# Kernel tuning notes

Measured on AMD Instinct MI355X. Metric: run time of the kernel, lower is better.

The kernel has to match this reference:

```python
import jax, jax.numpy as jnp
import numpy as np

N = 50000   # nodes
E = 800000  # edges (avg degree 16)
D = 256     # input = hidden = output dim
L = 3       # num_layers


def setup_inputs() -> dict:
    key = jax.random.key(0)
    k0, k1, k2, k3 = jax.random.split(key, 4)
    x = jax.random.normal(k0, (N, D), dtype=jnp.float32)
    edge_index = jax.random.randint(k1, (2, E), 0, N, dtype=jnp.int32)
    # SAGEConv params per layer: lin_l (neighbor path, with bias), lin_r (root path)
    Wl = jax.random.normal(k2, (L, D, D), dtype=jnp.float32) * 0.05
    Wr = jax.random.normal(k3, (L, D, D), dtype=jnp.float32) * 0.05
    b = jnp.zeros((L, D), dtype=jnp.float32)
    return {"x": x, "edge_index": edge_index, "Wl": Wl, "Wr": Wr, "b": b}


def reference(x, edge_index, Wl, Wr, b):
    src = edge_index[0]
    dst = edge_index[1]
    # in-degree for mean aggregation (clamped to avoid div-by-zero)
    deg = jax.ops.segment_sum(jnp.ones((E,), x.dtype), dst, num_segments=N)
    inv_deg = (1.0 / jnp.maximum(deg, 1.0))[:, None]  # [N,1]
    h = x
    for i in range(L):
        # gather source features, scatter-add into destinations, then mean
        agg = jax.ops.segment_sum(h[src], dst, num_segments=N) * inv_deg  # [N,D]
        h = agg @ Wl[i] + h @ Wr[i] + b[i]
        if i < L - 1:
            h = jax.nn.relu(h)  # dropout(p=0.1) is identity in eval mode
    return h
```

## Files before the change

### kernel.cpp

```cpp
#include <hip/hip_runtime.h>


typedef __attribute__((ext_vector_type(8))) _Float16 f16x8;
typedef __attribute__((ext_vector_type(4))) float f32x4;

__global__ void count_deg_kernel(const int* __restrict__ dst,
                                 int* __restrict__ deg, int E) {
    int i = (blockIdx.x * blockDim.x + threadIdx.x) * 2;
    if (i + 1 < E) {
        int2 d = *(const int2*)&dst[i];
        atomicAdd(&deg[d.x], 1);
        atomicAdd(&deg[d.y], 1);
    } else if (i < E) {
        atomicAdd(&deg[dst[i]], 1);
    }
}

__device__ __forceinline__ int block_excl_scan_256(int v, int tid) {
    int lane = tid & 63, w = tid >> 6;
    int x = v;
#pragma unroll
    for (int off = 1; off < 64; off <<= 1) {
        int y = __shfl_up(x, off);
        if (lane >= off) x += y;
    }
    __shared__ int wsum[4], woff[4];
    if (lane == 63) wsum[w] = x;
    __syncthreads();
    if (tid == 0) {
        int a = 0;
#pragma unroll
        for (int i = 0; i < 4; ++i) { woff[i] = a; a += wsum[i]; }
    }
    __syncthreads();
    return woff[w] + x - v;
}

__global__ void scan_phase1(const int* __restrict__ deg,
                            int* __restrict__ partial, int n) {
    int base = blockIdx.x * 1024;
    int s = 0;
    for (int i = threadIdx.x; i < 1024; i += 256) {
        int idx = base + i;
        s += (idx < n) ? deg[idx] : 0;
    }
    __shared__ int ws4[4];
    int lane = threadIdx.x & 63, w = threadIdx.x >> 6;
#pragma unroll
    for (int off = 32; off; off >>= 1) s += __shfl_down(s, off);
    if (lane == 0) ws4[w] = s;
    __syncthreads();
    if (threadIdx.x == 0)
        partial[blockIdx.x] = ws4[0] + ws4[1] + ws4[2] + ws4[3];
}

__global__ void scan_phase2(int* __restrict__ partial, int nb,
                            int* __restrict__ rowptr, int n, int E) {
    int tid = threadIdx.x;
    int v = (tid < nb) ? partial[tid] : 0;
    int ex = block_excl_scan_256(v, tid);
    if (tid < nb) partial[tid] = ex;
    if (tid == 0) rowptr[n] = E;
}

__global__ void scan_phase3(const int* __restrict__ deg,
                            const int* __restrict__ partial,
                            int* __restrict__ rowptr, int* __restrict__ cursor,
                            float* __restrict__ inv_deg, int n) {
    int base = blockIdx.x * 1024 + threadIdx.x * 4;
    int d[4];
#pragma unroll
    for (int j = 0; j < 4; ++j) {
        int idx = base + j;
        d[j] = (idx < n) ? deg[idx] : 0;
    }
    int tsum = d[0] + d[1] + d[2] + d[3];
    int ex = block_excl_scan_256(tsum, threadIdx.x);
    int run = partial[blockIdx.x] + ex;
#pragma unroll
    for (int j = 0; j < 4; ++j) {
        int idx = base + j;
        if (idx < n) {
            rowptr[idx] = run;
            cursor[idx] = run;
            inv_deg[idx] = 1.0f / (float)max(d[j], 1);
        }
        run += d[j];
    }
}

__global__ void fill_csr_kernel(const int* __restrict__ src,
                                const int* __restrict__ dst,
                                int* __restrict__ cursor,
                                int* __restrict__ csr_src, int E) {
    int i = (blockIdx.x * blockDim.x + threadIdx.x) * 2;
    if (i + 1 < E) {
        int2 d = *(const int2*)&dst[i];
        int2 s = *(const int2*)&src[i];
        int p0 = atomicAdd(&cursor[d.x], 1);
        csr_src[p0] = s.x;
        int p1 = atomicAdd(&cursor[d.y], 1);
        csr_src[p1] = s.y;
    } else if (i < E) {
        int p = atomicAdd(&cursor[dst[i]], 1);
        csr_src[p] = src[i];
    }
}

__global__ void presplit_w_kernel(const float* __restrict__ Wl,
                                  const float* __restrict__ Wr,
                                  _Float16* __restrict__ Wf,
                                  int* __restrict__ deg, int N, int total) {
    int idx = blockIdx.x * blockDim.x + threadIdx.x;
    if (idx < N) deg[idx] = 0;
    if (idx >= total) return;
    int l = idx >> 17;
    int rem = idx & 131071;
    int s = rem >> 16;
    int kc = rem & 65535;
    int k = kc >> 8, c = kc & 255;
    const float* W = s ? Wr : Wl;
    float w = W[((size_t)l * 256 + k) * 256 + c];
    int k0c = k >> 5, g = (k >> 3) & 3, j = k & 7;
    int tile = c >> 4, col = c & 15;
    int fi = (l * 2 + s) * 65536 + k0c * 8192 + ((tile * 4 + g) * 16 + col) * 8 + j;
    Wf[fi] = (_Float16)w;
}

__device__ __forceinline__ void gemm_from_lds64(
    const _Float16 (*Ah)[65][8], int tid, const _Float16* __restrict__ wbase,
    f16x8* blc, f16x8* brc, const float* __restrict__ bias,
    _Float16* __restrict__ zl, _Float16* __restrict__ zr, int r0, int M) {
    const int wave = tid >> 6, lane = tid & 63;
    const int l15 = lane & 15, lg = lane >> 4;
    const int wr = (wave & 1) * 32;
    const int wc = (wave >> 1) * 64;
    const int tg0 = wc >> 4;

    f32x4 accl[2][4], accr[2][4];
#pragma unroll
    for (int rt = 0; rt < 2; ++rt)
#pragma unroll
        for (int t = 0; t < 4; ++t) {
            accl[rt][t] = (f32x4)(0.0f);
            accr[rt][t] = (f32x4)(0.0f);
        }

#pragma unroll
    for (int s = 0; s < 8; ++s) {
        f16x8 bln[4], brn[4];
        if (s < 7) {
            const _Float16* wn = wbase + (s + 1) * 8192;
#pragma unroll
            for (int t = 0; t < 4; ++t) {
                bln[t] = *(const f16x8*)&wn[(tg0 + t) * 512];
                brn[t] = *(const f16x8*)&wn[65536 + (tg0 + t) * 512];
            }
        }
        f16x8 a0 = *(const f16x8*)&Ah[s * 4 + lg][wr + l15][0];
        f16x8 a1 = *(const f16x8*)&Ah[s * 4 + lg][wr + 16 + l15][0];
#pragma unroll
        for (int t = 0; t < 4; ++t) {
            accl[0][t] = __builtin_amdgcn_mfma_f32_16x16x32_f16(a0, blc[t],
                                                                accl[0][t], 0, 0, 0);
            accl[1][t] = __builtin_amdgcn_mfma_f32_16x16x32_f16(a1, blc[t],
                                                                accl[1][t], 0, 0, 0);
            accr[0][t] = __builtin_amdgcn_mfma_f32_16x16x32_f16(a0, brc[t],
                                                                accr[0][t], 0, 0, 0);
            accr[1][t] = __builtin_amdgcn_mfma_f32_16x16x32_f16(a1, brc[t],
                                                                accr[1][t], 0, 0, 0);
        }
        if (s < 7) {
#pragma unroll
            for (int t = 0; t < 4; ++t) {
                blc[t] = bln[t];
                brc[t] = brn[t];
            }
        }
    }

    float bv[4];
#pragma unroll
    for (int t = 0; t < 4; ++t) bv[t] = bias[wc + t * 16 + l15];
#pragma unroll
    for (int rt = 0; rt < 2; ++rt) {
#pragma unroll
        for (int r = 0; r < 4; ++r) {
            int grow = r0 + wr + rt * 16 + lg * 4 + r;
            if (grow >= M) continue;
#pragma unroll
            for (int t = 0; t < 4; ++t) {
                int col = wc + t * 16 + l15;
                int p = col >> 5, off = col & 31;
                size_t zi = ((size_t)p * M + grow) * 32 + off;
                zl[zi] = (_Float16)accl[rt][t][r];
                zr[zi] = (_Float16)(accr[rt][t][r] + bv[t]);
            }
        }
    }
}

__global__ __launch_bounds__(512) void gemm_dual_kernel(
    const float* __restrict__ xsrc, const _Float16* __restrict__ hsrc,
    int f32src, _Float16* __restrict__ zl, _Float16* __restrict__ zr,
    const _Float16* __restrict__ Wf_l, const float* __restrict__ bias, int M) {
    __shared__ __align__(16) _Float16 Ah[32][65][8];
    const int tid = threadIdx.x;
    const int r0 = blockIdx.x * 64;
    const int lane = tid & 63;
    const int l15 = lane & 15, lg = lane >> 4;
    const int tg0 = ((tid >> 6) >> 1) * 4;
    const _Float16* wbase = Wf_l + (lg * 16 + l15) * 8;

    f16x8 blc[4], brc[4];
#pragma unroll
    for (int t = 0; t < 4; ++t) {
        blc[t] = *(const f16x8*)&wbase[(tg0 + t) * 512];
        brc[t] = *(const f16x8*)&wbase[65536 + (tg0 + t) * 512];
    }

#pragma unroll
    for (int i = 0; i < 4; ++i) {
        int idx = i * 512 + tid;
        int row = idx >> 5, g = idx & 31;
        int grow = r0 + row;
        f16x8 v = (f16x8)(_Float16)0;
        if (grow < M) {
            if (f32src) {
                const float4* p =
                    (const float4*)&xsrc[(size_t)grow * 256 + g * 8];
                float4 v0 = p[0], v1 = p[1];
                v[0] = (_Float16)v0.x; v[1] = (_Float16)v0.y;
                v[2] = (_Float16)v0.z; v[3] = (_Float16)v0.w;
                v[4] = (_Float16)v1.x; v[5] = (_Float16)v1.y;
                v[6] = (_Float16)v1.z; v[7] = (_Float16)v1.w;
            } else {
                v = *(const f16x8*)&hsrc[(size_t)grow * 256 + g * 8];
            }
        }
        *(f16x8*)&Ah[g][row][0] = v;
    }
    __syncthreads();
    gemm_from_lds64(Ah, tid, wbase, blc, brc, bias, zl, zr, r0, M);
}

__global__ __launch_bounds__(256) void combine_panel_kernel(
    const _Float16* __restrict__ zl, const _Float16* __restrict__ zr,
    const int* __restrict__ rowptr, const int* __restrict__ csr_src,
    const float* __restrict__ inv_deg, _Float16* __restrict__ hout,
    float* __restrict__ fout, int n, int mode) {
    const int slice = blockIdx.x & 7;
    const int chunk = blockIdx.x >> 3;
    const int grp = threadIdx.x >> 3;
    const int sub = threadIdx.x & 7;
    const int pair = sub >> 2;
    const int l4 = sub & 3;
    const _Float16* zlp = zl + (size_t)slice * n * 32 + l4 * 8;
    const _Float16* zrp = zr + (size_t)slice * n * 32 + l4 * 8;

    int v = chunk * 32 + grp;
    if (v >= n) return;
    int beg = rowptr[v], end = rowptr[v + 1];
    float sc = inv_deg[v];
    float acc[8] = {0.f, 0.f, 0.f, 0.f, 0.f, 0.f, 0.f, 0.f};
    for (int e = beg; e < end; e += 16) {
        int e0 = e + pair * 8;
        f16x8 t[8];
#pragma unroll
        for (int k = 0; k < 8; ++k) {
            int ee = min(e0 + k, end - 1);
            int u = csr_src[ee];
            t[k] = *(const f16x8*)&zlp[(size_t)u * 32];
        }
#pragma unroll
        for (int k = 0; k < 8; ++k) {
            if (e0 + k < end) {
#pragma unroll
                for (int j = 0; j < 8; ++j) acc[j] += (float)t[k][j];
            }
        }
    }
#pragma unroll
    for (int j = 0; j < 8; ++j) acc[j] += __shfl_xor(acc[j], 4);
    if (pair == 0) {
        f16x8 zp = *(const f16x8*)&zrp[(size_t)v * 32];
        float o[8];
#pragma unroll
        for (int j = 0; j < 8; ++j) o[j] = acc[j] * sc + (float)zp[j];
        int cbase = slice * 32 + l4 * 8;
        if (mode == 0) {
            f16x8 hv;
#pragma unroll
            for (int j = 0; j < 8; ++j) hv[j] = (_Float16)fmaxf(o[j], 0.0f);
            *(f16x8*)&hout[(size_t)v * 256 + cbase] = hv;
        } else {
            float4* op = (float4*)&fout[(size_t)v * 256 + cbase];
            op[0] = make_float4(o[0], o[1], o[2], o[3]);
            op[1] = make_float4(o[4], o[5], o[6], o[7]);
        }
    }
}

extern "C" void kernel_launch(void* const* d_in, const int* in_sizes, int n_in,
                              void* d_out, int out_size, void* d_ws, size_t ws_size,
                              hipStream_t stream) {
    const int D = 256;
    const int N = in_sizes[0] / D;
    const int E = in_sizes[1] / 2;
    const int L = in_sizes[2] / (D * D);

    const float* x  = (const float*)d_in[0];
    const int*   ei = (const int*)d_in[1];
    const float* Wl = (const float*)d_in[2];
    const float* Wr = (const float*)d_in[3];
    const float* b  = (const float*)d_in[4];
    const int* src = ei;
    const int* dst = ei + E;

    size_t off = 0;
    auto alloc = [&](size_t bytes) {
        void* p = (char*)d_ws + off;
        off += (bytes + 255) & ~(size_t)255;
        return p;
    };
    int*   deg     = (int*)alloc((size_t)N * 4);
    int*   rowptr  = (int*)alloc((size_t)(N + 1) * 4);
    int*   cursor  = (int*)alloc((size_t)N * 4);
    float* inv_deg = (float*)alloc((size_t)N * 4);
    int*   csr_src = (int*)alloc((size_t)E * 4);
    int*   partial = (int*)alloc(256 * 4);
    _Float16* zlP  = (_Float16*)alloc((size_t)N * D * 2);
    _Float16* zrP  = (_Float16*)alloc((size_t)N * D * 2);
    _Float16* hbuf = (_Float16*)alloc((size_t)N * D * 2);
    _Float16* Wf   = (_Float16*)alloc((size_t)L * 2 * 65536 * 2);
    (void)ws_size;

    _Float16* zlQ = (_Float16*)d_out;
    _Float16* zrQ = zlQ + (size_t)N * D;
    float* outf = (float*)d_out;

    const int scan_blocks = (N + 1023) / 1024;

    int wtotal = L * 2 * 65536;
    hipLaunchKernelGGL(presplit_w_kernel, dim3((wtotal + 255) / 256), dim3(256),
                       0, stream, Wl, Wr, Wf, deg, N, wtotal);

    hipLaunchKernelGGL(count_deg_kernel, dim3((E / 2 + 255) / 256), dim3(256),
                       0, stream, dst, deg, E);
    hipLaunchKernelGGL(scan_phase1, dim3(scan_blocks), dim3(256), 0, stream,
                       deg, partial, N);
    hipLaunchKernelGGL(scan_phase2, dim3(1), dim3(256), 0, stream,
                       partial, scan_blocks, rowptr, N, E);
    hipLaunchKernelGGL(scan_phase3, dim3(scan_blocks), dim3(256), 0, stream,
                       deg, partial, rowptr, cursor, inv_deg, N);
    hipLaunchKernelGGL(fill_csr_kernel, dim3((E / 2 + 255) / 256), dim3(256),
                       0, stream, src, dst, cursor, csr_src, E);

    const int gemm_blocks = (N + 63) / 64;
    const int comb_blocks = 8 * ((N + 31) / 32);

    hipLaunchKernelGGL(gemm_dual_kernel, dim3(gemm_blocks), dim3(512), 0,
                       stream, x, (const _Float16*)nullptr, 1, zlP, zrP,
                       Wf, b, N);
    hipLaunchKernelGGL(combine_panel_kernel, dim3(comb_blocks), dim3(256), 0,
                       stream, zlP, zrP, rowptr, csr_src, inv_deg,
                       hbuf, outf, N, 0);
    hipLaunchKernelGGL(gemm_dual_kernel, dim3(gemm_blocks), dim3(512), 0,
                       stream, (const float*)nullptr, hbuf, 0, zlQ, zrQ,
                       Wf + 131072, b + D, N);
    hipLaunchKernelGGL(combine_panel_kernel, dim3(comb_blocks), dim3(256), 0,
                       stream, zlQ, zrQ, rowptr, csr_src, inv_deg,
                       hbuf, outf, N, 0);
    hipLaunchKernelGGL(gemm_dual_kernel, dim3(gemm_blocks), dim3(512), 0,
                       stream, (const float*)nullptr, hbuf, 0, zlP, zrP,
                       Wf + 262144, b + 2 * D, N);
    hipLaunchKernelGGL(combine_panel_kernel, dim3(comb_blocks), dim3(256), 0,
                       stream, zlP, zrP, rowptr, csr_src, inv_deg,
                       hbuf, outf, N, 1);
}
```

Measured before the change: 359.1 us.

## Stage GEMM outputs through LDS for coalesced stores; accumulate gathers in fp16

The GEMM epilogue now writes the lin_l and lin_r results into a padded shared-memory buffer and then stores them as 16-byte vectors per row panel, replacing scattered 2-byte global writes. The combine kernel sums the gathered neighbor rows in packed fp16 vectors instead of converting each to fp32. It drops the per-edge validity branch by always adding clamped duplicates and subtracting the extra copies of the last neighbor afterward. The fp16 accumulation lowers arithmetic cost but loses precision for high-degree nodes, and the subtraction trick adds its own rounding error.

After: 405.4 us. +12.9%, slower.

```diff
diff --git a/kernel.cpp b/kernel.cpp
--- a/kernel.cpp
+++ b/kernel.cpp
@@ -127,89 +127,20 @@
     Wf[fi] = (_Float16)w;
 }
 
-__device__ __forceinline__ void gemm_from_lds64(
-    const _Float16 (*Ah)[65][8], int tid, const _Float16* __restrict__ wbase,
-    f16x8* blc, f16x8* brc, const float* __restrict__ bias,
-    _Float16* __restrict__ zl, _Float16* __restrict__ zr, int r0, int M) {
+__global__ __launch_bounds__(512) void gemm_dual_kernel(
+    const float* __restrict__ xsrc, const _Float16* __restrict__ hsrc,
+    int f32src, _Float16* __restrict__ zl, _Float16* __restrict__ zr,
+    const _Float16* __restrict__ Wf_l, const float* __restrict__ bias, int M) {
+    __shared__ __align__(16) _Float16 Buf[18432];
+    _Float16 (*Ah)[65][8] = (_Float16(*)[65][8])Buf;
+
+    const int tid = threadIdx.x;
+    const int r0 = blockIdx.x * 64;
     const int wave = tid >> 6, lane = tid & 63;
     const int l15 = lane & 15, lg = lane >> 4;
     const int wr = (wave & 1) * 32;
     const int wc = (wave >> 1) * 64;
     const int tg0 = wc >> 4;
-
-    f32x4 accl[2][4], accr[2][4];
-#pragma unroll
-    for (int rt = 0; rt < 2; ++rt)
-#pragma unroll
-        for (int t = 0; t < 4; ++t) {
-            accl[rt][t] = (f32x4)(0.0f);
-            accr[rt][t] = (f32x4)(0.0f);
-        }
-
-#pragma unroll
-    for (int s = 0; s < 8; ++s) {
-        f16x8 bln[4], brn[4];
-        if (s < 7) {
-            const _Float16* wn = wbase + (s + 1) * 8192;
-#pragma unroll
-            for (int t = 0; t < 4; ++t) {
-                bln[t] = *(const f16x8*)&wn[(tg0 + t) * 512];
-                brn[t] = *(const f16x8*)&wn[65536 + (tg0 + t) * 512];
-            }
-        }
-        f16x8 a0 = *(const f16x8*)&Ah[s * 4 + lg][wr + l15][0];
-        f16x8 a1 = *(const f16x8*)&Ah[s * 4 + lg][wr + 16 + l15][0];
-#pragma unroll
-        for (int t = 0; t < 4; ++t) {
-            accl[0][t] = __builtin_amdgcn_mfma_f32_16x16x32_f16(a0, blc[t],
-                                                                accl[0][t], 0, 0, 0);
-            accl[1][t] = __builtin_amdgcn_mfma_f32_16x16x32_f16(a1, blc[t],
-                                                                accl[1][t], 0, 0, 0);
-            accr[0][t] = __builtin_amdgcn_mfma_f32_16x16x32_f16(a0, brc[t],
-                                                                accr[0][t], 0, 0, 0);
-            accr[1][t] = __builtin_amdgcn_mfma_f32_16x16x32_f16(a1, brc[t],
-                                                                accr[1][t], 0, 0, 0);
-        }
-        if (s < 7) {
-#pragma unroll
-            for (int t = 0; t < 4; ++t) {
-                blc[t] = bln[t];
-                brc[t] = brn[t];
-            }
-        }
-    }
-
-    float bv[4];
-#pragma unroll
-    for (int t = 0; t < 4; ++t) bv[t] = bias[wc + t * 16 + l15];
-#pragma unroll
-    for (int rt = 0; rt < 2; ++rt) {
-#pragma unroll
-        for (int r = 0; r < 4; ++r) {
-            int grow = r0 + wr + rt * 16 + lg * 4 + r;
-            if (grow >= M) continue;
-#pragma unroll
-            for (int t = 0; t < 4; ++t) {
-                int col = wc + t * 16 + l15;
-                int p = col >> 5, off = col & 31;
-                size_t zi = ((size_t)p * M + grow) * 32 + off;
-                zl[zi] = (_Float16)accl[rt][t][r];
-                zr[zi] = (_Float16)(accr[rt][t][r] + bv[t]);
-            }
-        }
-    }
-}
-
-__global__ __launch_bounds__(512) void gemm_dual_kernel(
-    const float* __restrict__ xsrc, const _Float16* __restrict__ hsrc,
-    int f32src, _Float16* __restrict__ zl, _Float16* __restrict__ zr,
-    const _Float16* __restrict__ Wf_l, const float* __restrict__ bias, int M) {
-    __shared__ __align__(16) _Float16 Ah[32][65][8];
-    const int tid = threadIdx.x;
-    const int r0 = blockIdx.x * 64;
-    const int lane = tid & 63;
-    const int l15 = lane & 15, lg = lane >> 4;
-    const int tg0 = ((tid >> 6) >> 1) * 4;
     const _Float16* wbase = Wf_l + (lg * 16 + l15) * 8;
 
     f16x8 blc[4], brc[4];
@@ -241,7 +172,84 @@
         *(f16x8*)&Ah[g][row][0] = v;
     }
     __syncthreads();
-    gemm_from_lds64(Ah, tid, wbase, blc, brc, bias, zl, zr, r0, M);
+
+    f32x4 accl[2][4], accr[2][4];
+#pragma unroll
+    for (int rt = 0; rt < 2; ++rt)
+#pragma unroll
+        for (int t = 0; t < 4; ++t) {
+            accl[rt][t] = (f32x4)(0.0f);
+            accr[rt][t] = (f32x4)(0.0f);
+        }
+
+#pragma unroll
+    for (int s = 0; s < 8; ++s) {
+        f16x8 bln[4], brn[4];
+        if (s < 7) {
+            const _Float16* wn = wbase + (s + 1) * 8192;
+#pragma unroll
+            for (int t = 0; t < 4; ++t) {
+                bln[t] = *(const f16x8*)&wn[(tg0 + t) * 512];
+                brn[t] = *(const f16x8*)&wn[65536 + (tg0 + t) * 512];
+            }
+        }
+        f16x8 a0 = *(const f16x8*)&Ah[s * 4 + lg][wr + l15][0];
+        f16x8 a1 = *(const f16x8*)&Ah[s * 4 + lg][wr + 16 + l15][0];
+#pragma unroll
+        for (int t = 0; t < 4; ++t) {
+            accl[0][t] = __builtin_amdgcn_mfma_f32_16x16x32_f16(a0, blc[t],
+                                                                accl[0][t], 0, 0, 0);
+            accl[1][t] = __builtin_amdgcn_mfma_f32_16x16x32_f16(a1, blc[t],
+                                                                accl[1][t], 0, 0, 0);
+            accr[0][t] = __builtin_amdgcn_mfma_f32_16x16x32_f16(a0, brc[t],
+                                                                accr[0][t], 0, 0, 0);
+            accr[1][t] = __builtin_amdgcn_mfma_f32_16x16x32_f16(a1, brc[t],
+                                                                accr[1][t], 0, 0, 0);
+        }
+        if (s < 7) {
+#pragma unroll
+            for (int t = 0; t < 4; ++t) {
+                blc[t] = bln[t];
+                brc[t] = brn[t];
+            }
+        }
+    }
+
+    float bv[4];
+#pragma unroll
+    for (int t = 0; t < 4; ++t) bv[t] = bias[wc + t * 16 + l15];
+
+#pragma unroll
+    for (int ph = 0; ph < 2; ++ph) {
+        __syncthreads();
+#pragma unroll
+        for (int rt = 0; rt < 2; ++rt)
+#pragma unroll
+            for (int r = 0; r < 4; ++r) {
+                int row = wr + rt * 16 + lg * 4 + r;
+#pragma unroll
+                for (int t = 0; t < 4; ++t) {
+                    int col = wc + t * 16 + l15;
+                    int p = col >> 5, off = col & 31;
+                    float val = ph ? (accr[rt][t][r] + bv[t])
+                                   : accl[rt][t][r];
+                    Buf[(p * 64 + row) * 36 + off] = (_Float16)val;
+                }
+            }
+        __syncthreads();
+        _Float16* zout = ph ? zr : zl;
+#pragma unroll
+        for (int i = 0; i < 4; ++i) {
+            int u = i * 512 + tid;
+            int p = u >> 8;
+            int rr = (u & 255) >> 2;
+            int ui = u & 3;
+            f16x8 vv = *(const f16x8*)&Buf[(p * 64 + rr) * 36 + ui * 8];
+            int grow = r0 + rr;
+            if (grow < M)
+                *(f16x8*)&zout[((size_t)p * M + grow) * 32 + ui * 8] = vv;
+        }
+    }
 }
 
 __global__ __launch_bounds__(256) void combine_panel_kernel(
@@ -262,31 +270,41 @@
     if (v >= n) return;
     int beg = rowptr[v], end = rowptr[v + 1];
     float sc = inv_deg[v];
-    float acc[8] = {0.f, 0.f, 0.f, 0.f, 0.f, 0.f, 0.f, 0.f};
-    for (int e = beg; e < end; e += 16) {
-        int e0 = e + pair * 8;
-        f16x8 t[8];
-#pragma unroll
-        for (int k = 0; k < 8; ++k) {
-            int ee = min(e0 + k, end - 1);
-            int u = csr_src[ee];
-            t[k] = *(const f16x8*)&zlp[(size_t)u * 32];
-        }
-#pragma unroll
-        for (int k = 0; k < 8; ++k) {
-            if (e0 + k < end) {
-#pragma unroll
-                for (int j = 0; j < 8; ++j) acc[j] += (float)t[k][j];
-            }
-        }
-    }
-#pragma unroll
-    for (int j = 0; j < 8; ++j) acc[j] += __shfl_xor(acc[j], 4);
+    float o[8];
+    if (beg < end) {
+        f16x8 acch = (f16x8)(_Float16)0;
+        for (int e = beg; e < end; e += 16) {
+            int e0 = e + pair * 8;
+            f16x8 t[8];
+#pragma unroll
+            for (int k = 0; k < 8; ++k) {
+                int ee = min(e0 + k, end - 1);
+                int u = csr_src[ee];
+                t[k] = *(const f16x8*)&zlp[(size_t)u * 32];
+            }
+#pragma unroll
+            for (int k = 0; k < 8; ++k) acch += t[k];
+        }
+        int d = end - beg;
+        int T = (d + 15) >> 4;
+        int rem = d - ((T - 1) << 4);
+        int valid = pair ? max(rem - 8, 0) : min(rem, 8);
+        float inval = (float)(8 - valid);
+        int ulast = csr_src[end - 1];
+        f16x8 tl = *(const f16x8*)&zlp[(size_t)ulast * 32];
+#pragma unroll
+        for (int j = 0; j < 8; ++j)
+            o[j] = (float)acch[j] - inval * (float)tl[j];
+    } else {
+#pragma unroll
+        for (int j = 0; j < 8; ++j) o[j] = 0.0f;
+    }
+#pragma unroll
+    for (int j = 0; j < 8; ++j) o[j] += __shfl_xor(o[j], 4);
     if (pair == 0) {
         f16x8 zp = *(const f16x8*)&zrp[(size_t)v * 32];
-        float o[8];
-#pragma unroll
-        for (int j = 0; j < 8; ++j) o[j] = acc[j] * sc + (float)zp[j];
+#pragma unroll
+        for (int j = 0; j < 8; ++j) o[j] = o[j] * sc + (float)zp[j];
         int cbase = slice * 32 + l4 * 8;
         if (mode == 0) {
             f16x8 hv;
```
